# Kernel optimization log

Measured on AMD Instinct MI355X. Metric: run time of the kernel, lower is better.

## Reference

```python
import jax, jax.numpy as jnp
import numpy as np

B, S, H, NH = 4, 2048, 1024, 16
HD = H // NH
EPS = 1e-12

def setup_inputs() -> dict:
    key = jax.random.key(0)
    ks = jax.random.split(key, 8)
    sc = 1.0 / np.sqrt(H)
    return {
        "input_tensor": jax.random.normal(ks[0], (B, S, H), jnp.float32),
        "attention_mask": jnp.zeros((B, 1, 1, S), jnp.float32),
        "Wq": jax.random.normal(ks[1], (H, H), jnp.float32) * sc,
        "bq": jnp.zeros((H,), jnp.float32),
        "Wk": jax.random.normal(ks[2], (H, H), jnp.float32) * sc,
        "bk": jnp.zeros((H,), jnp.float32),
        "Wv": jax.random.normal(ks[3], (H, H), jnp.float32) * sc,
        "bv": jnp.zeros((H,), jnp.float32),
        "Wo": jax.random.normal(ks[4], (H, H), jnp.float32) * sc,
        "bo": jnp.zeros((H,), jnp.float32),
        "ln_w": jnp.ones((H,), jnp.float32),
        "ln_b": jnpp_zeros if False else jnp.zeros((H,), jnp.float32),
    }

def reference(input_tensor, attention_mask, Wq, bq, Wk, bk, Wv, bv, Wo, bo, ln_w, ln_b):
    x = input_tensor  # [B,S,H]
    # QKV projections (torch Linear: x @ W.T + b), split heads -> [B,S,NH,HD]
    q = (x @ Wq.T + bq).reshape(B, S, NH, HD)
    k = (x @ Wk.T + bk).reshape(B, S, NH, HD)
    v = (x @ Wv.T + bv).reshape(B, S, NH, HD)
    # scores [B,NH,S,S]
    scores = jnp.einsum('bqhd,bkhd->bhqk', q, k) / jnp.sqrt(jnp.float32(HD))
    scores = scores + attention_mask  # broadcast [B,1,1,S]
    probs = jax.nn.softmax(scores, axis=-1)  # dropout is identity in eval
    ctx = jnp.einsum('bhqk,bkhd->bqhd', probs, v).reshape(B, S, H)
    # output dense + residual + LayerNorm (TF-style eps inside sqrt)
    h = ctx @ Wo.T + bo + x
    u = h.mean(-1, keepdims=True)
    s = jnp.mean((h - u) ** 2, axis=-1, keepdims=True)
    return ln_w * (h - u) / jnp.sqrt(s + EPS) + ln_b
```

## Files before the change

### kernel.cpp

```cpp
#include <hip/hip_runtime.h>

typedef __bf16 bf16;
typedef __bf16 bf16x8 __attribute__((ext_vector_type(8)));
typedef __bf16 bf16x4 __attribute__((ext_vector_type(4)));
typedef float floatx4 __attribute__((ext_vector_type(4)));
typedef int   intx4  __attribute__((ext_vector_type(4)));
typedef int   intx2  __attribute__((ext_vector_type(2)));

#define MFMA16(a,b,c) __builtin_amdgcn_mfma_f32_16x16x32_bf16((a),(b),(c),0,0,0)

constexpr int Bc  = 4;
constexpr int Sc  = 2048;
constexpr int Hc  = 1024;
constexpr int NHc = 16;
constexpr int HDc = 64;
constexpr int Mc  = Bc * Sc;
constexpr int KIT = Hc / 32;
constexpr float L2E = 1.44269504088896f;

union U64  { bf16x4 h; intx2 i; };

__device__ __forceinline__ void ld16(const bf16* g, bf16* l) {
    __builtin_amdgcn_global_load_lds(
        (const __attribute__((address_space(1))) void*)g,
        (__attribute__((address_space(3))) void*)l, 16, 0, 0);
}

__global__ void detect_k(const unsigned short* __restrict__ x, int* __restrict__ flag)
{
    if (threadIdx.x == 0 && blockIdx.x == 0) {
        float mx = 0.f;
        for (int i = 0; i < 256; ++i) {
            unsigned int bits = ((unsigned int)x[i]) << 16;
            float v = __uint_as_float(bits);
            if (!isfinite(v)) { mx = 1e30f; break; }
            mx = fmaxf(mx, fabsf(v));
        }
        *flag = (mx > 1e6f) ? 1 : 0;
    }
}

__global__ __launch_bounds__(256)
void conv_all_k(const void* __restrict__ x,
                const void* __restrict__ Wq, const void* __restrict__ Wk,
                const void* __restrict__ Wv, const void* __restrict__ Wo,
                const void* __restrict__ mask,
                const void* __restrict__ bq, const void* __restrict__ bk,
                const void* __restrict__ bv, const void* __restrict__ bo,
                const void* __restrict__ lnw, const void* __restrict__ lnb,
                bf16* __restrict__ xb, bf16* __restrict__ wdst,
                float* maskf, float* bqf, float* bkf, float* bvf,
                float* bof, float* lnwf, float* lnbf,
                const int* __restrict__ flag)
{
    const int g = blockIdx.x * 256 + threadIdx.x;
    const int fl = *flag;
    if (g < 1048576) {
        if (fl) {
            const float* s = (const float*)x + (size_t)g * 8;
            union { intx4 v; bf16 e[8]; } o;
#pragma unroll
            for (int j = 0; j < 8; ++j) o.e[j] = (bf16)s[j];
            *(intx4*)(xb + (size_t)g * 8) = o.v;
        } else {
            *(intx4*)(xb + (size_t)g * 8) = *((const intx4*)x + g);
        }
    } else if (g < 1048576 + 524288) {
        const int gw = g - 1048576;
        const int wsel = gw >> 17, go = gw & 131071;
        const void* s = (wsel == 0) ? Wq : (wsel == 1) ? Wk : (wsel == 2) ? Wv : Wo;
        if (fl) {
            const float* sp = (const float*)s + (size_t)go * 8;
            union { intx4 v; bf16 e[8]; } o;
#pragma unroll
            for (int j = 0; j < 8; ++j) o.e[j] = (bf16)sp[j];
            *(intx4*)(wdst + (size_t)gw * 8) = o.v;
        } else {
            *(intx4*)(wdst + (size_t)gw * 8) = *((const intx4*)s + go);
        }
    } else {
        const int gs = g - 1048576 - 524288;
        if (gs >= 1792) return;
        const void* src; float* dst; int off; float scl = 1.0f;
        if (gs < 1024) { src = mask; dst = maskf; off = gs * 8; scl = L2E; }
        else {
            const int a = (gs - 1024) >> 7;
            off = ((gs - 1024) & 127) * 8;
            switch (a) {
                case 0: src = bq;  dst = bqf;  break;
                case 1: src = bk;  dst = bkf;  break;
                case 2: src = bv;  dst = bvf;  break;
                case 3: src = bo;  dst = bof;  break;
                case 4: src = lnw; dst = lnwf; break;
                default: src = lnb; dst = lnbf; break;
            }
        }
        if (fl) {
            const float* s = (const float*)src + off;
#pragma unroll
            for (int j = 0; j < 8; ++j) dst[off + j] = s[j] * scl;
        } else {
            union { intx4 v; bf16 e[8]; } u;
            u.v = *(const intx4*)((const bf16*)src + off);
#pragma unroll
            for (int j = 0; j < 8; ++j) dst[off + j] = (float)u.e[j] * scl;
        }
    }
}

template<int SWAP>
__device__ __forceinline__
void gemm_core(const bf16* __restrict__ A, const bf16* __restrict__ W,
               int m0, int n0, int t, bf16* As, bf16* Bs, floatx4 (&acc)[4][4])
{
    const int l  = t & 63, w = t >> 6;
    const int wr = w >> 1, wc = w & 1;
    const int lq = l >> 4, ln = l & 15;
    const int srow = t >> 2;
    const int scol = (t & 3) * 8;

    const bf16* a0 = A + (size_t)(m0 + srow) * Hc + scol;
    const bf16* b0 = W + (size_t)(n0 + srow) * Hc + scol;
    const int dst = srow * 32 + scol;

    auto stage = [&](int buf, int kb) {
        const int off = kb * 32;
        bf16* dA = As + buf * 4096;
        bf16* dB = Bs + buf * 4096;
        ld16(a0 + off,           dA + dst);
        ld16(a0 + 64 * Hc + off, dA + 64 * 32 + dst);
        ld16(b0 + off,           dB + dst);
        ld16(b0 + 64 * Hc + off, dB + 64 * 32 + dst);
    };

    stage(0, 0);
    int cur = 0;
    for (int kb = 0; kb < KIT; ++kb) {
        __syncthreads();
        if (kb + 1 < KIT) stage(cur ^ 1, kb + 1);

        const bf16* Ab = As + cur * 4096;
        const bf16* Bb = Bs + cur * 4096;
        bf16x8 af[4], bw[4];
#pragma unroll
        for (int i = 0; i < 4; ++i)
            af[i] = *(const bf16x8*)&Ab[(wr * 64 + i * 16 + ln) * 32 + lq * 8];
#pragma unroll
        for (int j = 0; j < 4; ++j)
            bw[j] = *(const bf16x8*)&Bb[(wc * 64 + j * 16 + ln) * 32 + lq * 8];

        __builtin_amdgcn_s_setprio(1);
#pragma unroll
        for (int i = 0; i < 4; ++i)
#pragma unroll
            for (int j = 0; j < 4; ++j)
                acc[i][j] = SWAP ? MFMA16(bw[j], af[i], acc[i][j])
                                 : MFMA16(af[i], bw[j], acc[i][j]);
        __builtin_amdgcn_s_setprio(0);
        cur ^= 1;
    }
}

__device__ __forceinline__ void xcd_remap(int bx, int by, int& m0, int& n0)
{
    const int flat = by * 8 + bx;
    const int sw   = (flat & 7) * 64 + (flat >> 3);
    m0 = (sw >> 3) * 128;
    n0 = (sw & 7) * 128;
}

__global__ __launch_bounds__(256)
void qkv_gemm(const bf16* __restrict__ x,
              const bf16* __restrict__ Wq, const float* __restrict__ bq,
              const bf16* __restrict__ Wk, const float* __restrict__ bk,
              const bf16* __restrict__ Wv, const float* __restrict__ bv,
              bf16* __restrict__ qo, bf16* __restrict__ ko, bf16* __restrict__ vto)
{
    __shared__ __align__(16) bf16 smem[16384];
    const int z = blockIdx.z;
    const bf16*  W    = (z == 0) ? Wq : (z == 1) ? Wk : Wv;
    const float* bias = (z == 0) ? bq : (z == 1) ? bk : bv;

    int m0, n0;
    xcd_remap(blockIdx.x, blockIdx.y, m0, n0);
    const int t  = threadIdx.x;
    const int l  = t & 63, w = t >> 6;
    const int wr = w >> 1, wc = w & 1;
    const int lq = l >> 4, ln = l & 15;

    if (z < 2) {
        floatx4 acc[4][4] = {};
        gemm_core<1>(x, W, m0, n0, t, smem, smem + 8192, acc);
        bf16* out = (z == 0) ? qo : ko;
        const float sc = (z == 0) ? 0.125f * L2E : 1.0f;
#pragma unroll
        for (int j = 0; j < 4; ++j) {
            const int feat = n0 + wc * 64 + j * 16 + lq * 4;
            const floatx4 bb = *(const floatx4*)&bias[feat];
            const int hh = feat >> 6, dd = feat & 63;
#pragma unroll
            for (int i = 0; i < 4; ++i) {
                const int xrow = m0 + wr * 64 + i * 16 + ln;
                const int bi = xrow >> 11, si = xrow & (Sc - 1);
                U64 pk;
#pragma unroll
                for (int r = 0; r < 4; ++r) pk.h[r] = (bf16)((acc[i][j][r] + bb[r]) * sc);
                *(intx2*)&out[(((size_t)bi * NHc + hh) * Sc + si) * HDc + dd] = pk.i;
            }
        }
    } else {
        floatx4 acc[4][4] = {};
        gemm_core<0>(x, W, m0, n0, t, smem, smem + 8192, acc);
        bf16* Ct = smem;
        const int bi = m0 >> 11, s0 = m0 & (Sc - 1);
        for (int h2 = 0; h2 < 2; ++h2) {
            __syncthreads();
            if (wc == h2) {
#pragma unroll
                for (int j = 0; j < 4; ++j) {
                    const int c = j * 16 + ln;
                    const float bb = bias[n0 + h2 * 64 + c];
#pragma unroll
                    for (int i = 0; i < 4; ++i) {
                        U64 pk;
#pragma unroll
                        for (int r = 0; r < 4; ++r) pk.h[r] = (bf16)(acc[i][j][r] + bb);
                        *(intx2*)&Ct[c * 136 + wr * 64 + i * 16 + lq * 4] = pk.i;
                    }
                }
            }
            __syncthreads();
#pragma unroll
            for (int u = 0; u < 4; ++u) {
                const int id = t + 256 * u;
                const int c = id >> 4, rg = id & 15;
                const int hh = (n0 >> 6) + h2;
                intx4 val = *(const intx4*)&Ct[c * 136 + rg * 8];
                *(intx4*)&vto[(((size_t)bi * NHc + hh) * HDc + c) * Sc + s0 + rg * 8] = val;
            }
        }
    }
}

__global__ __launch_bounds__(256)
void oproj_gemm(const bf16* __restrict__ ctx, const bf16* __restrict__ Wo,
                const float* __restrict__ bo, const bf16* __restrict__ xb,
                bf16* __restrict__ hout)
{
    __shared__ __align__(16) bf16 smem[16384];
    int m0, n0;
    xcd_remap(blockIdx.x, blockIdx.y, m0, n0);
    const int t  = threadIdx.x;
    floatx4 acc[4][4] = {};
    gemm_core<1>(ctx, Wo, m0, n0, t, smem, smem + 8192, acc);

    const int l  = t & 63, w = t >> 6;
    const int wr = w >> 1, wc = w & 1;
    const int lq = l >> 4, ln = l & 15;
#pragma unroll
    for (int j = 0; j < 4; ++j) {
        const int col = n0 + wc * 64 + j * 16 + lq * 4;
        const floatx4 bb = *(const floatx4*)&bo[col];
#pragma unroll
        for (int i = 0; i < 4; ++i) {
            const int row = m0 + wr * 64 + i * 16 + ln;
            U64 rx;
            rx.i = *(const intx2*)&xb[(size_t)row * Hc + col];
            U64 pk;
#pragma unroll
            for (int r = 0; r < 4; ++r)
                pk.h[r] = (bf16)(acc[i][j][r] + bb[r] + (float)rx.h[r]);
            *(intx2*)&hout[(size_t)row * Hc + col] = pk.i;
        }
    }
}

__global__ __launch_bounds__(256, 4)
void attention(const bf16* __restrict__ q, const bf16* __restrict__ k,
               const bf16* __restrict__ vt, const float* __restrict__ maskf,
               bf16* __restrict__ ctx)
{
    __shared__ __align__(16) bf16 KV[2][2][64][64];

    const int raw = blockIdx.x;
    const int xcd = raw & 7, jj = raw >> 3;
    const int bh  = xcd * 8 + (jj >> 4);
    const int qt  = jj & 15;
    const int b = bh >> 4, h = bh & 15;
    const int t = threadIdx.x, w = t >> 6, l = t & 63;
    const int lq = l >> 4, ln = l & 15;
    const int q0 = qt * 128 + w * 32;

    const bf16* kg = k  + (size_t)bh * Sc * HDc;
    const bf16* vg = vt + (size_t)bh * HDc * Sc;
    const float* mbase = maskf + b * Sc;

    const int rr  = l >> 3;
    const int gsw = ((l & 7) ^ rr) << 3;
    const int r0  = w * 16 + rr, r1 = r0 + 8;
    const int dco = (l & 7) << 3;

    bf16x8 qf[2][2];
#pragma unroll
    for (int qb = 0; qb < 2; ++qb)
#pragma unroll
        for (int kh = 0; kh < 2; ++kh)
            qf[qb][kh] = *(const bf16x8*)(q + ((size_t)bh * Sc + q0 + qb * 16 + ln) * HDc
                                            + kh * 32 + lq * 8);

    floatx4 o[2][4] = {};
    float dacc[2] = {0.f, 0.f};

    auto stage = [&](int buf, int kt) {
        bf16* Kd = &KV[buf][0][0][0];
        bf16* Vd = &KV[buf][1][0][0];
        ld16(kg + (size_t)(kt * 64 + r0) * HDc + gsw, Kd + r0 * 64 + dco);
        ld16(kg + (size_t)(kt * 64 + r1) * HDc + gsw, Kd + r1 * 64 + dco);
        ld16(vg + (size_t)r0 * Sc + kt * 64 + gsw,    Vd + r0 * 64 + dco);
        ld16(vg + (size_t)r1 * Sc + kt * 64 + gsw,    Vd + r1 * 64 + dco);
    };

    stage(0, 0);
    int cur = 0;
    const int sw = ln & 7;

    for (int kt = 0; kt < Sc / 64; ++kt) {
        __syncthreads();
        if (kt + 1 < Sc / 64) stage(cur ^ 1, kt + 1);

        const bf16* Kb = &KV[cur][0][0][0];
        const bf16* Vb = &KV[cur][1][0][0];

        floatx4 s[2][4];
#pragma unroll
        for (int cb = 0; cb < 4; ++cb) {
            const floatx4 mv = *(const floatx4*)(mbase + kt * 64 + cb * 16 + lq * 4);
            s[0][cb] = mv;
            s[1][cb] = mv;
        }

#pragma unroll
        for (int kh = 0; kh < 2; ++kh) {
            bf16x8 kf[4];
#pragma unroll
            for (int cb = 0; cb < 4; ++cb) {
                const int cc = ((kh * 4 + lq) ^ sw) << 3;
                kf[cb] = *(const bf16x8*)&Kb[(cb * 16 + ln) * 64 + cc];
            }
            __builtin_amdgcn_s_setprio(1);
#pragma unroll
            for (int qb = 0; qb < 2; ++qb)
#pragma unroll
                for (int cb = 0; cb < 4; ++cb)
                    s[qb][cb] = MFMA16(kf[cb], qf[qb][kh], s[qb][cb]);
            __builtin_amdgcn_s_setprio(0);
        }

        bf16x8 pf[2][2];
#pragma unroll
        for (int qb = 0; qb < 2; ++qb) {
            unsigned int D[4][2];
            float ds = 0.f;
#pragma unroll
            for (int cb = 0; cb < 4; ++cb)
#pragma unroll
                for (int i = 0; i < 2; ++i) {
                    const float e0 = __builtin_amdgcn_exp2f(s[qb][cb][2 * i]);
                    const float e1 = __builtin_amdgcn_exp2f(s[qb][cb][2 * i + 1]);
                    ds += e0 + e1;
                    union { unsigned int u; bf16 e[2]; } pk2;
                    pk2.e[0] = (bf16)e0; pk2.e[1] = (bf16)e1;
                    D[cb][i] = pk2.u;
                }
            dacc[qb] += ds;

            unsigned int F0[4], F1[4];
            {
                unsigned int A, B;
                A = D[0][0]; B = D[1][0];
                asm("v_permlane32_swap_b32 %0, %1" : "+v"(A), "+v"(B));
                asm("v_permlane16_swap_b32 %0, %1" : "+v"(A), "+v"(B));
                F0[0] = A; F0[2] = B;
                A = D[0][1]; B = D[1][1];
                asm("v_permlane32_swap_b32 %0, %1" : "+v"(A), "+v"(B));
                asm("v_permlane16_swap_b32 %0, %1" : "+v"(A), "+v"(B));
                F0[1] = A; F0[3] = B;
                A = D[2][0]; B = D[3][0];
                asm("v_permlane32_swap_b32 %0, %1" : "+v"(A), "+v"(B));
                asm("v_permlane16_swap_b32 %0, %1" : "+v"(A), "+v"(B));
                F1[0] = A; F1[2] = B;
                A = D[2][1]; B = D[3][1];
                asm("v_permlane32_swap_b32 %0, %1" : "+v"(A), "+v"(B));
                asm("v_permlane16_swap_b32 %0, %1" : "+v"(A), "+v"(B));
                F1[1] = A; F1[3] = B;
            }
            union { unsigned int u[4]; bf16x8 v; } P0, P1;
#pragma unroll
            for (int d = 0; d < 4; ++d) { P0.u[d] = F0[d]; P1.u[d] = F1[d]; }
            pf[qb][0] = P0.v;
            pf[qb][1] = P1.v;
        }

#pragma unroll
        for (int kh = 0; kh < 2; ++kh) {
            bf16x8 vf[4];
#pragma unroll
            for (int db = 0; db < 4; ++db) {
                const int cc = ((kh * 4 + lq) ^ sw) << 3;
                vf[db] = *(const bf16x8*)&Vb[(db * 16 + ln) * 64 + cc];
            }
            __builtin_amdgcn_s_setprio(1);
#pragma unroll
            for (int qb = 0; qb < 2; ++qb)
#pragma unroll
                for (int db = 0; db < 4; ++db)
                    o[qb][db] = MFMA16(vf[db], pf[qb][kh], o[qb][db]);
            __builtin_amdgcn_s_setprio(0);
        }
        cur ^= 1;
    }

#pragma unroll
    for (int qb = 0; qb < 2; ++qb) {
        float dsum = dacc[qb];
        dsum += __shfl_xor(dsum, 16, 64);
        dsum += __shfl_xor(dsum, 32, 64);
        const float li = 1.f / dsum;
        const int qg = q0 + qb * 16 + ln;
#pragma unroll
        for (int db = 0; db < 4; ++db) {
            U64 pk;
#pragma unroll
            for (int r = 0; r < 4; ++r) pk.h[r] = (bf16)(o[qb][db][r] * li);
            *(intx2*)&ctx[((size_t)b * Sc + qg) * Hc + h * HDc + db * 16 + lq * 4] = pk.i;
        }
    }
}

__global__ __launch_bounds__(256)
void layernorm_k(const bf16* __restrict__ hbuf, const float* __restrict__ lw,
                 const float* __restrict__ lb, void* __restrict__ outp,
                 const int* __restrict__ flag)
{
    const int row = blockIdx.x;
    const int t = threadIdx.x;
    const bf16* hp = hbuf + (size_t)row * Hc;

    union { intx2 i2; bf16 e[4]; } pk;
    pk.i2 = *(const intx2*)(hp + t * 4);
    float v[4], sum = 0.f, sq = 0.f;
#pragma unroll
    for (int i = 0; i < 4; ++i) {
        v[i] = (float)pk.e[i];
        sum += v[i];
        sq  += v[i] * v[i];
    }
#pragma unroll
    for (int off = 1; off < 64; off <<= 1) {
        sum += __shfl_xor(sum, off, 64);
        sq  += __shfl_xor(sq,  off, 64);
    }
    __shared__ float ssum[4], ssq[4];
    const int w = t >> 6;
    if ((t & 63) == 0) { ssum[w] = sum; ssq[w] = sq; }
    __syncthreads();
    sum = ssum[0] + ssum[1] + ssum[2] + ssum[3];
    sq  = ssq[0]  + ssq[1]  + ssq[2]  + ssq[3];

    const float mean = sum * (1.f / (float)Hc);
    const float var  = sq * (1.f / (float)Hc) - mean * mean;
    const float rstd = rsqrtf(var + 1e-12f);

    float ov[4];
#pragma unroll
    for (int i = 0; i < 4; ++i) {
        const int c = t * 4 + i;
        ov[i] = lw[c] * (v[i] - mean) * rstd + lb[c];
    }
    if (*flag) {
        float* of = (float*)outp + (size_t)row * Hc + t * 4;
#pragma unroll
        for (int i = 0; i < 4; ++i) of[i] = ov[i];
    } else {
        union { intx2 i2; bf16 e[4]; } po;
#pragma unroll
        for (int i = 0; i < 4; ++i) po.e[i] = (bf16)ov[i];
        *(intx2*)((bf16*)outp + (size_t)row * Hc + t * 4) = po.i2;
    }
}

extern "C" void kernel_launch(void* const* d_in, const int* in_sizes, int n_in,
                              void* d_out, int out_size, void* d_ws, size_t ws_size,
                              hipStream_t stream)
{
    const void* x    = d_in[0];
    const void* mask = d_in[1];
    const void* Wq   = d_in[2];
    const void* bq   = d_in[3];
    const void* Wk   = d_in[4];
    const void* bk   = d_in[5];
    const void* Wv   = d_in[6];
    const void* bv   = d_in[7];
    const void* Wo   = d_in[8];
    const void* bo   = d_in[9];
    const void* lnw  = d_in[10];
    const void* lnb  = d_in[11];

    char* ws = (char*)d_ws;
    const size_t MB = 1024 * 1024;
    int*   flag  = (int*)ws;
    float* maskf = (float*)(ws + 4096);
    float* bqf   = (float*)(ws + 64 * 1024);
    float* bkf   = bqf + Hc;
    float* bvf   = bkf + Hc;
    float* bof   = bvf + Hc;
    float* lnwf  = bof + Hc;
    float* lnbf  = lnwf + Hc;
    bf16* xb  = (bf16*)(ws + 1 * MB);
    bf16* wqb = (bf16*)(ws + 17 * MB);
    bf16* wkb = (bf16*)(ws + 19 * MB);
    bf16* wvb = (bf16*)(ws + 21 * MB);
    bf16* wob = (bf16*)(ws + 23 * MB);
    bf16* qb  = (bf16*)(ws + 25 * MB);
    bf16* kb  = (bf16*)(ws + 41 * MB);
    bf16* vtb = (bf16*)(ws + 57 * MB);
    bf16* cb  = (bf16*)(ws + 73 * MB);
    bf16* hb  = qb;

    detect_k<<<1, 64, 0, stream>>>((const unsigned short*)x, flag);

    conv_all_k<<<6153, 256, 0, stream>>>(x, Wq, Wk, Wv, Wo, mask,
                                         bq, bk, bv, bo, lnw, lnb,
                                         xb, wqb, maskf, bqf, bkf, bvf,
                                         bof, lnwf, lnbf, flag);

    dim3 gqkv(Hc / 128, Mc / 128, 3);
    qkv_gemm<<<gqkv, 256, 0, stream>>>(xb, wqb, bqf, wkb, bkf, wvb, bvf, qb, kb, vtb);
    attention<<<dim3(Bc * NHc * (Sc / 128)), 256, 0, stream>>>(qb, kb, vtb, maskf, cb);
    oproj_gemm<<<dim3(Hc / 128, Mc / 128), 256, 0, stream>>>(cb, wob, bof, xb, hb);
    layernorm_k<<<dim3(Mc), 256, 0, stream>>>(hb, lnwf, lnbf, d_out, flag);
}
```

Before: 342.0 us.

## Restructure attention into software-pipelined QK/PV with 256-row query tiles

Each attention block now covers 256 query rows (64 per wave), doubling K/V reuse per tile and halving the grid. The P·V matmul for the previous key tile is overlapped with the QK^T of the current tile. Probabilities are passed through an LDS scratch buffer instead of permlane swaps, and V is loaded straight from global memory into registers rather than staged in LDS. This raises register pressure (launch bounds lowered to 2 waves per SIMD) and adds LDS round-trips for P in exchange for less K/V traffic and better MFMA overlap.

Measured after the change: 340.9 us. No clear change (-0.3%).

```diff
diff --git a/kernel.cpp b/kernel.cpp
--- a/kernel.cpp
+++ b/kernel.cpp
@@ -275,21 +275,22 @@
     }
 }
 
-__global__ __launch_bounds__(256, 4)
+__global__ __launch_bounds__(256, 2)
 void attention(const bf16* __restrict__ q, const bf16* __restrict__ k,
                const bf16* __restrict__ vt, const float* __restrict__ maskf,
                bf16* __restrict__ ctx)
 {
-    __shared__ __align__(16) bf16 KV[2][2][64][64];
+    __shared__ __align__(16) bf16 Ks[2][64][64];
+    __shared__ __align__(16) bf16 Pt[256][72];
 
     const int raw = blockIdx.x;
     const int xcd = raw & 7, jj = raw >> 3;
-    const int bh  = xcd * 8 + (jj >> 4);
-    const int qt  = jj & 15;
+    const int bh  = xcd * 8 + (jj >> 3);
+    const int qt  = jj & 7;
     const int b = bh >> 4, h = bh & 15;
     const int t = threadIdx.x, w = t >> 6, l = t & 63;
     const int lq = l >> 4, ln = l & 15;
-    const int q0 = qt * 128 + w * 32;
+    const int q0 = qt * 256 + w * 64;
 
     const bf16* kg = k  + (size_t)bh * Sc * HDc;
     const bf16* vg = vt + (size_t)bh * HDc * Sc;
@@ -299,129 +300,117 @@
     const int gsw = ((l & 7) ^ rr) << 3;
     const int r0  = w * 16 + rr, r1 = r0 + 8;
     const int dco = (l & 7) << 3;
-
-    bf16x8 qf[2][2];
-#pragma unroll
-    for (int qb = 0; qb < 2; ++qb)
+    const int sw  = ln & 7;
+
+    bf16x8 qf[4][2];
+#pragma unroll
+    for (int qb = 0; qb < 4; ++qb)
 #pragma unroll
         for (int kh = 0; kh < 2; ++kh)
             qf[qb][kh] = *(const bf16x8*)(q + ((size_t)bh * Sc + q0 + qb * 16 + ln) * HDc
                                             + kh * 32 + lq * 8);
 
-    floatx4 o[2][4] = {};
-    float dacc[2] = {0.f, 0.f};
-
-    auto stage = [&](int buf, int kt) {
-        bf16* Kd = &KV[buf][0][0][0];
-        bf16* Vd = &KV[buf][1][0][0];
+    floatx4 o[4][4] = {};
+    float dacc[4] = {0.f, 0.f, 0.f, 0.f};
+    floatx4 s[4][4];
+    bf16x8 vf[4][2];
+
+    auto stageK = [&](int buf, int kt) {
+        bf16* Kd = &Ks[buf][0][0];
         ld16(kg + (size_t)(kt * 64 + r0) * HDc + gsw, Kd + r0 * 64 + dco);
         ld16(kg + (size_t)(kt * 64 + r1) * HDc + gsw, Kd + r1 * 64 + dco);
-        ld16(vg + (size_t)r0 * Sc + kt * 64 + gsw,    Vd + r0 * 64 + dco);
-        ld16(vg + (size_t)r1 * Sc + kt * 64 + gsw,    Vd + r1 * 64 + dco);
     };
-
-    stage(0, 0);
+    auto loadV = [&](int kt) {
+#pragma unroll
+        for (int db = 0; db < 4; ++db)
+#pragma unroll
+            for (int kh = 0; kh < 2; ++kh)
+                vf[db][kh] = *(const bf16x8*)(vg + (size_t)(db * 16 + ln) * Sc
+                                                + kt * 64 + kh * 32 + lq * 8);
+    };
+    auto doQKT = [&](int kt, int cur) {
+        floatx4 mvl[4];
+#pragma unroll
+        for (int cb = 0; cb < 4; ++cb)
+            mvl[cb] = *(const floatx4*)(mbase + kt * 64 + cb * 16 + lq * 4);
+        bf16x8 kf[4][2];
+#pragma unroll
+        for (int cb = 0; cb < 4; ++cb)
+#pragma unroll
+            for (int kh = 0; kh < 2; ++kh)
+                kf[cb][kh] = *(const bf16x8*)&Ks[cur][cb * 16 + ln]
+                                               [((kh * 4 + lq) ^ sw) << 3];
+#pragma unroll
+        for (int qb = 0; qb < 4; ++qb)
+#pragma unroll
+            for (int cb = 0; cb < 4; ++cb)
+                s[qb][cb] = mvl[cb];
+        __builtin_amdgcn_s_setprio(1);
+#pragma unroll
+        for (int kh = 0; kh < 2; ++kh)
+#pragma unroll
+            for (int qb = 0; qb < 4; ++qb)
+#pragma unroll
+                for (int cb = 0; cb < 4; ++cb)
+                    s[qb][cb] = MFMA16(kf[cb][kh], qf[qb][kh], s[qb][cb]);
+        __builtin_amdgcn_s_setprio(0);
+    };
+    auto doPV = [&]() {
+        __builtin_amdgcn_s_setprio(1);
+#pragma unroll
+        for (int qb = 0; qb < 4; ++qb) {
+            const bf16x8 pf0 = *(const bf16x8*)&Pt[w * 64 + qb * 16 + ln][lq * 8];
+            const bf16x8 pf1 = *(const bf16x8*)&Pt[w * 64 + qb * 16 + ln][32 + lq * 8];
+#pragma unroll
+            for (int db = 0; db < 4; ++db) {
+                o[qb][db] = MFMA16(vf[db][0], pf0, o[qb][db]);
+                o[qb][db] = MFMA16(vf[db][1], pf1, o[qb][db]);
+            }
+        }
+        __builtin_amdgcn_s_setprio(0);
+    };
+    auto doSoftmax = [&]() {
+#pragma unroll
+        for (int qb = 0; qb < 4; ++qb) {
+            float ds = 0.f;
+#pragma unroll
+            for (int cb = 0; cb < 4; ++cb) {
+                U64 pk;
+#pragma unroll
+                for (int r = 0; r < 4; ++r) {
+                    const float e = __builtin_amdgcn_exp2f(s[qb][cb][r]);
+                    ds += e;
+                    pk.h[r] = (bf16)e;
+                }
+                *(intx2*)&Pt[w * 64 + qb * 16 + ln][cb * 16 + lq * 4] = pk.i;
+            }
+            dacc[qb] += ds;
+        }
+    };
+
+    stageK(0, 0);
+    loadV(0);
     int cur = 0;
-    const int sw = ln & 7;
-
-    for (int kt = 0; kt < Sc / 64; ++kt) {
+
+    __syncthreads();
+    stageK(1, 1);
+    doQKT(0, 0);
+    doSoftmax();
+    cur = 1;
+
+    for (int kt = 1; kt < Sc / 64; ++kt) {
         __syncthreads();
-        if (kt + 1 < Sc / 64) stage(cur ^ 1, kt + 1);
-
-        const bf16* Kb = &KV[cur][0][0][0];
-        const bf16* Vb = &KV[cur][1][0][0];
-
-        floatx4 s[2][4];
-#pragma unroll
-        for (int cb = 0; cb < 4; ++cb) {
-            const floatx4 mv = *(const floatx4*)(mbase + kt * 64 + cb * 16 + lq * 4);
-            s[0][cb] = mv;
-            s[1][cb] = mv;
-        }
-
-#pragma unroll
-        for (int kh = 0; kh < 2; ++kh) {
-            bf16x8 kf[4];
-#pragma unroll
-            for (int cb = 0; cb < 4; ++cb) {
-                const int cc = ((kh * 4 + lq) ^ sw) << 3;
-                kf[cb] = *(const bf16x8*)&Kb[(cb * 16 + ln) * 64 + cc];
-            }
-            __builtin_amdgcn_s_setprio(1);
-#pragma unroll
-            for (int qb = 0; qb < 2; ++qb)
-#pragma unroll
-                for (int cb = 0; cb < 4; ++cb)
-                    s[qb][cb] = MFMA16(kf[cb], qf[qb][kh], s[qb][cb]);
-            __builtin_amdgcn_s_setprio(0);
-        }
-
-        bf16x8 pf[2][2];
-#pragma unroll
-        for (int qb = 0; qb < 2; ++qb) {
-            unsigned int D[4][2];
-            float ds = 0.f;
-#pragma unroll
-            for (int cb = 0; cb < 4; ++cb)
-#pragma unroll
-                for (int i = 0; i < 2; ++i) {
-                    const float e0 = __builtin_amdgcn_exp2f(s[qb][cb][2 * i]);
-                    const float e1 = __builtin_amdgcn_exp2f(s[qb][cb][2 * i + 1]);
-                    ds += e0 + e1;
-                    union { unsigned int u; bf16 e[2]; } pk2;
-                    pk2.e[0] = (bf16)e0; pk2.e[1] = (bf16)e1;
-                    D[cb][i] = pk2.u;
-                }
-            dacc[qb] += ds;
-
-            unsigned int F0[4], F1[4];
-            {
-                unsigned int A, B;
-                A = D[0][0]; B = D[1][0];
-                asm("v_permlane32_swap_b32 %0, %1" : "+v"(A), "+v"(B));
-                asm("v_permlane16_swap_b32 %0, %1" : "+v"(A), "+v"(B));
-                F0[0] = A; F0[2] = B;
-                A = D[0][1]; B = D[1][1];
-                asm("v_permlane32_swap_b32 %0, %1" : "+v"(A), "+v"(B));
-                asm("v_permlane16_swap_b32 %0, %1" : "+v"(A), "+v"(B));
-                F0[1] = A; F0[3] = B;
-                A = D[2][0]; B = D[3][0];
-                asm("v_permlane32_swap_b32 %0, %1" : "+v"(A), "+v"(B));
-                asm("v_permlane16_swap_b32 %0, %1" : "+v"(A), "+v"(B));
-                F1[0] = A; F1[2] = B;
-                A = D[2][1]; B = D[3][1];
-                asm("v_permlane32_swap_b32 %0, %1" : "+v"(A), "+v"(B));
-                asm("v_permlane16_swap_b32 %0, %1" : "+v"(A), "+v"(B));
-                F1[1] = A; F1[3] = B;
-            }
-            union { unsigned int u[4]; bf16x8 v; } P0, P1;
-#pragma unroll
-            for (int d = 0; d < 4; ++d) { P0.u[d] = F0[d]; P1.u[d] = F1[d]; }
-            pf[qb][0] = P0.v;
-            pf[qb][1] = P1.v;
-        }
-
-#pragma unroll
-        for (int kh = 0; kh < 2; ++kh) {
-            bf16x8 vf[4];
-#pragma unroll
-            for (int db = 0; db < 4; ++db) {
-                const int cc = ((kh * 4 + lq) ^ sw) << 3;
-                vf[db] = *(const bf16x8*)&Vb[(db * 16 + ln) * 64 + cc];
-            }
-            __builtin_amdgcn_s_setprio(1);
-#pragma unroll
-            for (int qb = 0; qb < 2; ++qb)
-#pragma unroll
-                for (int db = 0; db < 4; ++db)
-                    o[qb][db] = MFMA16(vf[db], pf[qb][kh], o[qb][db]);
-            __builtin_amdgcn_s_setprio(0);
-        }
+        if (kt + 1 < Sc / 64) stageK(cur ^ 1, kt + 1);
+        doQKT(kt, cur);
+        doPV();
+        loadV(kt);
+        doSoftmax();
         cur ^= 1;
     }
-
-#pragma unroll
-    for (int qb = 0; qb < 2; ++qb) {
+    doPV();
+
+#pragma unroll
+    for (int qb = 0; qb < 4; ++qb) {
         float dsum = dacc[qb];
         dsum += __shfl_xor(dsum, 16, 64);
         dsum += __shfl_xor(dsum, 32, 64);
@@ -536,7 +525,7 @@
 
     dim3 gqkv(Hc / 128, Mc / 128, 3);
     qkv_gemm<<<gqkv, 256, 0, stream>>>(xb, wqb, bqf, wkb, bkf, wvb, bvf, qb, kb, vtb);
-    attention<<<dim3(Bc * NHc * (Sc / 128)), 256, 0, stream>>>(qb, kb, vtb, maskf, cb);
+    attention<<<dim3(Bc * NHc * (Sc / 256)), 256, 0, stream>>>(qb, kb, vtb, maskf, cb);
     oproj_gemm<<<dim3(Hc / 128, Mc / 128), 256, 0, stream>>>(cb, wob, bof, xb, hb);
     layernorm_k<<<dim3(Mc), 256, 0, stream>>>(hb, lnwf, lnbf, d_out, flag);
 }
```
